# Performance work log

Hardware: AMD Instinct MI355X
Metric: run time of the kernel (lower is better)

## Reference

```python
import jax, jax.numpy as jnp
import numpy as np

B = 256      # number of graphs
IN = 128     # input_dim
FD = 256     # feature_dim (dims[1])
HID = 256    # hidden_dim of attention block (dims[2])
OUT = 128    # final output dim (dims[3])
TXT = 512    # text_emb_dim

LENGTHS = np.asarray(128 + (np.arange(B) % 256), dtype=np.int64)  # ragged lens 128..383
N = int(LENGTHS.sum())  # 65408 total nodes
LMAX = int(LENGTHS.max())  # 383


def setup_inputs() -> dict:
    key = jax.random.key(0)
    ks = jax.random.split(key, 16)
    s = 0.02
    return {
        "input": jax.random.normal(ks[0], (N, IN), jnp.float32),
        "text_emb": jax.random.normal(ks[1], (B, TXT), jnp.float32),
        "repeat_list": jnp.asarray(LENGTHS),
        # layer 0: Linear(IN -> FD)
        "W0": jax.random.normal(ks[2], (IN, FD), jnp.float32) * s,
        "b0": jax.random.normal(ks[3], (FD,), jnp.float32) * s,
        # cross-attention block params
        "Wq": jax.random.normal(ks[4], (TXT, FD), jnp.float32) * s,
        "bq": jax.random.normal(ks[5], (FD,), jnp.float32) * s,
        "Wk": jax.random.normal(ks[6], (FD, FD), jnp.float32) * s,
        "bk": jax.random.normal(ks[7], (FD,), jnp.float32) * s,
        "Wv": jax.random.normal(ks[8], (FD, FD), jnp.float32) * s,
        "bv": jax.random.normal(ks[9], (FD,), jnp.float32) * s,
        "Wo": jax.random.normal(ks[10], (FD, HID), jnp.float32) * s,
        "bo": jax.random.normal(ks[11], (HID,), jnp.float32) * s,
        # layer 2: Linear(HID -> OUT), last layer (no activation)
        "W2": jax.random.normal(ks[12], (HID, OUT), jnp.float32) * s,
        "b2": jax.random.normal(ks[13], (OUT,), jnp.float32) * s,
    }


def _cross_attention(h, text_emb, repeat_list, Wq, bq, Wk, bk, Wv, bv, Wo, bo):
    # h: [N, FD] packed ragged node features; repeat_list: [B] lengths (constant ints)
    n = h.shape[0]
    b = repeat_list.shape[0]
    fd = h.shape[1]
    # pad ragged -> [B, LMAX, FD] (pad value 0) + validity mask
    seg = jnp.repeat(jnp.arange(b), repeat_list, total_repeat_length=n)  # [N] graph id
    offsets = jnp.cumsum(repeat_list) - repeat_list                      # [B] start of each graph
    pos = jnp.arange(n) - offsets[seg]                                   # [N] within-graph pos
    padded = jnp.zeros((b, LMAX, fd), h.dtype).at[seg, pos].set(h)
    valid = jnp.arange(LMAX)[None, :] < repeat_list[:, None]             # [B, L]

    q = text_emb @ Wq + bq                              # [B, FD]
    k = (padded @ Wk + bk) * valid[..., None]           # masked_fill(mask==0, 0)
    v = (padded @ Wv + bv) * valid[..., None]

    # query is broadcast identically over the padded-length axis, so each row of the
    # [L, L] score matrix is the same vector: scores[b, j] = q[b] . k[b, j]
    scores = jnp.einsum('bf,bjf->bj', q, k)             # [B, L]
    scores = jnp.where(valid, scores, -jnp.inf)         # mask invalid columns j
    p = jax.nn.softmax(scores, axis=-1)                 # [B, L]
    # output = attention^T @ value with identical rows => out[b,j,:] = p[b,j] * sum_i v[b,i,:]
    v_sum = v.sum(axis=1)                               # [B, FD] (padded rows already zero)
    out_pad = p[..., None] * v_sum[:, None, :]          # [B, L, FD]
    out_nodes = out_pad[seg, pos]                       # unpad-concat -> [N, FD]
    return out_nodes @ Wo + bo                          # [N, HID]


def reference(input, text_emb, repeat_list, W0, b0, Wq, bq, Wk, bk, Wv, bv, Wo, bo, W2, b2):
    h = jax.nn.relu(input @ W0 + b0)                                     # layer 0 + relu
    h = _cross_attention(h, text_emb, repeat_list, Wq, bq, Wk, bk, Wv, bv, Wo, bo)
    h = jax.nn.relu(h)                                                   # layer 1 + relu
    return h @ W2 + b2                                                   # layer 2 (last, no act)
```

## Files before the change

### kernel.cpp

```cpp
#include <hip/hip_runtime.h>
#include <math.h>

#define B_G   256
#define IN_D  128
#define FD    256
#define HID   256
#define OUT_D 128
#define TXT   512
#define XKS   136

typedef short bf16x8 __attribute__((ext_vector_type(8)));
typedef float f32x4  __attribute__((ext_vector_type(4)));

__device__ __forceinline__ unsigned bf_rne(float x) {
    unsigned u = __float_as_uint(x);
    u += 0x7fffu + ((u >> 16) & 1u);
    return u >> 16;
}
__device__ __forceinline__ float bf_to_f(unsigned h) {
    return __uint_as_float(h << 16);
}
__device__ __forceinline__ void split2(float a0, float a1, unsigned& hp, unsigned& lp) {
    unsigned h0 = bf_rne(a0), h1 = bf_rne(a1);
    float r0 = a0 - bf_to_f(h0), r1 = a1 - bf_to_f(h1);
    hp = h0 | (h1 << 16);
    lp = bf_rne(r0) | (bf_rne(r1) << 16);
}

__global__ __launch_bounds__(256) void k_prepA(
    const float* __restrict__ text_emb, const float* __restrict__ Wq,
    const float* __restrict__ bq, const float* __restrict__ Wk,
    const float* __restrict__ W0, const float* __restrict__ W2,
    const int* __restrict__ lens,
    float* __restrict__ qk, int* __restrict__ offsets, float* __restrict__ hsum,
    unsigned short* __restrict__ W0sH, unsigned short* __restrict__ W0sL,
    unsigned short* __restrict__ W2sH, unsigned short* __restrict__ W2sL)
{
    int blk = blockIdx.x, t = threadIdx.x;
    __shared__ float te[TXT];
    __shared__ float q[FD];
    __shared__ int   sc[B_G];

    if (blk < 256) {
        int b = blk;
        hsum[b * FD + t] = 0.f;
        for (int i = t; i < TXT; i += 256) te[i] = text_emb[(size_t)b * TXT + i];
        __syncthreads();
        float acc = bq[t];
        for (int k = 0; k < TXT; k++) acc = fmaf(te[k], Wq[k * FD + t], acc);
        q[t] = acc;
        __syncthreads();
        float a2 = 0.f;
        for (int f = 0; f < FD; f++) a2 = fmaf(Wk[t * FD + f], q[f], a2);
        qk[b * FD + t] = a2;
    } else if (blk < 264) {
        int e = (blk - 256) * 256 + t;
        if (e < 1024) {
            int kc = e >> 8, c = e & 255;
            size_t base = (size_t)(kc * 256 + c) * 32;
            for (int kk = 0; kk < 32; kk++) {
                float v = W0[(size_t)(kc * 32 + kk) * FD + c];
                unsigned h = bf_rne(v);
                float r = v - bf_to_f(h);
                W0sH[base + kk] = (unsigned short)h;
                W0sL[base + kk] = (unsigned short)bf_rne(r);
            }
        } else {
            int e2 = e - 1024;
            int kc = e2 >> 7, c = e2 & 127;
            size_t base = (size_t)(kc * 128 + c) * 32;
            for (int kk = 0; kk < 32; kk++) {
                float v = W2[(size_t)(kc * 32 + kk) * OUT_D + c];
                unsigned h = bf_rne(v);
                float r = v - bf_to_f(h);
                W2sH[base + kk] = (unsigned short)h;
                W2sL[base + kk] = (unsigned short)bf_rne(r);
            }
        }
    } else {
        sc[t] = lens[t];
        __syncthreads();
        for (int d = 1; d < 256; d <<= 1) {
            int v = (t >= d) ? sc[t - d] : 0;
            __syncthreads();
            sc[t] += v;
            __syncthreads();
        }
        offsets[t + 1] = sc[t];
        if (t == 0) offsets[0] = 0;
    }
}

__global__ __launch_bounds__(256, 4) void k_l0_mfma(
    const float* __restrict__ X,
    const unsigned short* __restrict__ W0sH, const unsigned short* __restrict__ W0sL,
    const float* __restrict__ b0, const float* __restrict__ qk,
    const int* __restrict__ offsets,
    float* __restrict__ scores, float* __restrict__ hsum)
{
    int b = blockIdx.y;
    int off = offsets[b], len = offsets[b + 1] - off;
    int n0 = blockIdx.x * 64;
    if (n0 >= len) return;
    int nvalid = min(64, len - n0);

    __shared__ __align__(16) unsigned short XsH[64 * XKS], XsL[64 * XKS];
    __shared__ float qks[FD];
    __shared__ float bsh[FD];
    __shared__ float red[4][64];

    int tid = threadIdx.x;
    int lane = tid & 63, w = tid >> 6;
    int ln = lane & 15, quad = lane >> 4;

    qks[tid] = qk[b * FD + tid];
    bsh[tid] = b0[tid];

    {
        int node_s = tid >> 2, ks = (tid & 3) * 32;
        const float4* Xr4 = (const float4*)(X + (size_t)(off + n0 + node_s) * IN_D + ks);
        bool v = (node_s < nvalid);
#pragma unroll
        for (int g = 0; g < 4; g++) {
            float4 a, c4;
            if (v) { a = Xr4[2 * g]; c4 = Xr4[2 * g + 1]; }
            else   { a = make_float4(0.f, 0.f, 0.f, 0.f); c4 = a; }
            uint4 hq, lq;
            split2(a.x,  a.y,  hq.x, lq.x);
            split2(a.z,  a.w,  hq.y, lq.y);
            split2(c4.x, c4.y, hq.z, lq.z);
            split2(c4.z, c4.w, hq.w, lq.w);
            *(uint4*)&XsH[node_s * XKS + ks + g * 8] = hq;
            *(uint4*)&XsL[node_s * XKS + ks + g * 8] = lq;
        }
    }
    __syncthreads();

    f32x4 acc[4][4] = {};
#pragma unroll
    for (int kc = 0; kc < 4; kc++) {
        bf16x8 AH[4], AL[4];
#pragma unroll
        for (int i = 0; i < 4; i++) {
            AH[i] = *(const bf16x8*)&XsH[(16 * i + ln) * XKS + kc * 32 + quad * 8];
            AL[i] = *(const bf16x8*)&XsL[(16 * i + ln) * XKS + kc * 32 + quad * 8];
        }
#pragma unroll
        for (int j = 0; j < 4; j++) {
            int c = 64 * w + 16 * j + ln;
            size_t base = (size_t)(kc * 256 + c) * 32 + quad * 8;
            bf16x8 BH = *(const bf16x8*)&W0sH[base];
            bf16x8 BL = *(const bf16x8*)&W0sL[base];
#pragma unroll
            for (int i = 0; i < 4; i++) {
                acc[i][j] = __builtin_amdgcn_mfma_f32_16x16x32_bf16(AH[i], BH, acc[i][j], 0, 0, 0);
                acc[i][j] = __builtin_amdgcn_mfma_f32_16x16x32_bf16(AH[i], BL, acc[i][j], 0, 0, 0);
                acc[i][j] = __builtin_amdgcn_mfma_f32_16x16x32_bf16(AL[i], BH, acc[i][j], 0, 0, 0);
            }
        }
    }

    float sp[4][4];
    float cs[4] = {0.f, 0.f, 0.f, 0.f};
#pragma unroll
    for (int i = 0; i < 4; i++)
#pragma unroll
        for (int r = 0; r < 4; r++) sp[i][r] = 0.f;

#pragma unroll
    for (int i = 0; i < 4; i++)
#pragma unroll
        for (int j = 0; j < 4; j++) {
            int c = 64 * w + 16 * j + ln;
            float bb = bsh[c], qv = qks[c];
#pragma unroll
            for (int r = 0; r < 4; r++) {
                int node = 16 * i + 4 * quad + r;
                float h = acc[i][j][r] + bb;
                h = (h > 0.f && node < nvalid) ? h : 0.f;
                sp[i][r] = fmaf(h, qv, sp[i][r]);
                cs[j] += h;
            }
        }
#pragma unroll
    for (int i = 0; i < 4; i++)
#pragma unroll
        for (int r = 0; r < 4; r++) {
            float s = sp[i][r];
            s += __shfl_xor(s, 1); s += __shfl_xor(s, 2);
            s += __shfl_xor(s, 4); s += __shfl_xor(s, 8);
            sp[i][r] = s;
        }
    if (ln == 0) {
#pragma unroll
        for (int i = 0; i < 4; i++)
#pragma unroll
            for (int r = 0; r < 4; r++)
                red[w][16 * i + 4 * quad + r] = sp[i][r];
    }
#pragma unroll
    for (int j = 0; j < 4; j++) {
        float s = cs[j];
        s += __shfl_xor(s, 16); s += __shfl_xor(s, 32);
        if (quad == 0) atomicAdd(&hsum[b * FD + 64 * w + 16 * j + ln], s);
    }
    __syncthreads();
    if (tid < 64 && tid < nvalid)
        scores[off + n0 + tid] = red[0][tid] + red[1][tid] + red[2][tid] + red[3][tid];
}

__global__ __launch_bounds__(1024) void k_graph(
    const float* __restrict__ scores, const float* __restrict__ hsum,
    const float* __restrict__ Wv, const float* __restrict__ bv,
    const float* __restrict__ Wo, const int* __restrict__ offsets,
    float* __restrict__ wvec, float* __restrict__ smax, float* __restrict__ dinv)
{
    int b = blockIdx.x, tid = threadIdx.x;
    int t = tid & 255, g = tid >> 8;
    int off = offsets[b], len = offsets[b + 1] - off;
    __shared__ float redm[16], reds[16];
    __shared__ float hs[FD], vs[FD];
    __shared__ float part[4][FD];

    float m = -INFINITY;
    for (int i = tid; i < len; i += 1024) m = fmaxf(m, scores[off + i]);
    for (int d = 1; d < 64; d <<= 1) m = fmaxf(m, __shfl_xor(m, d));
    if ((tid & 63) == 0) redm[tid >> 6] = m;
    __syncthreads();
    m = -INFINITY;
#pragma unroll
    for (int k = 0; k < 16; k++) m = fmaxf(m, redm[k]);

    float s = 0.f;
    for (int i = tid; i < len; i += 1024) s += expf(scores[off + i] - m);
    for (int d = 1; d < 64; d <<= 1) s += __shfl_xor(s, d);
    if ((tid & 63) == 0) reds[tid >> 6] = s;
    if (g == 0) hs[t] = hsum[b * FD + t];
    __syncthreads();
    s = 0.f;
#pragma unroll
    for (int k = 0; k < 16; k++) s += reds[k];

    float acc = (g == 0) ? (float)len * bv[t] : 0.f;
    for (int f = 64 * g; f < 64 * g + 64; f++) acc = fmaf(hs[f], Wv[f * FD + t], acc);
    part[g][t] = acc;
    __syncthreads();
    if (g == 0) vs[t] = part[0][t] + part[1][t] + part[2][t] + part[3][t];
    __syncthreads();
    float a2 = 0.f;
    for (int f = 64 * g; f < 64 * g + 64; f++) a2 = fmaf(vs[f], Wo[f * HID + t], a2);
    part[g][t] = a2;
    __syncthreads();
    if (g == 0) wvec[b * HID + t] = part[0][t] + part[1][t] + part[2][t] + part[3][t];
    if (tid == 0) { smax[b] = m; dinv[b] = 1.0f / s; }
}

__global__ __launch_bounds__(256, 4) void k_fin_mfma(
    const float* __restrict__ scores, const float* __restrict__ wvec,
    const float* __restrict__ bo,
    const unsigned short* __restrict__ W2sH, const unsigned short* __restrict__ W2sL,
    const float* __restrict__ b2, const float* __restrict__ smax,
    const float* __restrict__ dinv, const int* __restrict__ offsets,
    float* __restrict__ Y)
{
    int b = blockIdx.y;
    int off = offsets[b], len = offsets[b + 1] - off;
    int n0 = blockIdx.x * 64;
    if (n0 >= len) return;
    int nvalid = min(64, len - n0);

    int tid = threadIdx.x;
    int lane = tid & 63, w = tid >> 6;
    int ln = lane & 15, quad = lane >> 4;

    __shared__ __align__(16) unsigned short ZsH[64 * XKS], ZsL[64 * XKS];
    __shared__ float ps[64];
    __shared__ float wsh[HID];
    __shared__ float bosh[HID];
    __shared__ float b2sh[OUT_D];

    wsh[tid] = wvec[b * HID + tid];
    bosh[tid] = bo[tid];
    if (tid < OUT_D) b2sh[tid] = b2[tid];
    if (tid < 64) {
        float p = 0.f;
        if (tid < nvalid) p = expf(scores[off + n0 + tid] - smax[b]) * dinv[b];
        ps[tid] = p;
    }
    __syncthreads();

    f32x4 acc[4][2] = {};
    int node_s = tid >> 2, ks = (tid & 3) * 32;

#pragma unroll
    for (int h = 0; h < 2; h++) {
        if (h) __syncthreads();
        {
            float pn = ps[node_s];
            int kg0 = h * 128 + ks;
#pragma unroll
            for (int g = 0; g < 4; g++) {
                uint4 hq, lq;
                int kb = kg0 + g * 8;
                float z0, z1;
                z0 = fmaxf(fmaf(pn, wsh[kb + 0], bosh[kb + 0]), 0.f);
                z1 = fmaxf(fmaf(pn, wsh[kb + 1], bosh[kb + 1]), 0.f);
                split2(z0, z1, hq.x, lq.x);
                z0 = fmaxf(fmaf(pn, wsh[kb + 2], bosh[kb + 2]), 0.f);
                z1 = fmaxf(fmaf(pn, wsh[kb + 3], bosh[kb + 3]), 0.f);
                split2(z0, z1, hq.y, lq.y);
                z0 = fmaxf(fmaf(pn, wsh[kb + 4], bosh[kb + 4]), 0.f);
                z1 = fmaxf(fmaf(pn, wsh[kb + 5], bosh[kb + 5]), 0.f);
                split2(z0, z1, hq.z, lq.z);
                z0 = fmaxf(fmaf(pn, wsh[kb + 6], bosh[kb + 6]), 0.f);
                z1 = fmaxf(fmaf(pn, wsh[kb + 7], bosh[kb + 7]), 0.f);
                split2(z0, z1, hq.w, lq.w);
                *(uint4*)&ZsH[node_s * XKS + ks + g * 8] = hq;
                *(uint4*)&ZsL[node_s * XKS + ks + g * 8] = lq;
            }
        }
        __syncthreads();

#pragma unroll
        for (int kc = 0; kc < 4; kc++) {
            bf16x8 AH[4], AL[4];
#pragma unroll
            for (int i = 0; i < 4; i++) {
                AH[i] = *(const bf16x8*)&ZsH[(16 * i + ln) * XKS + kc * 32 + quad * 8];
                AL[i] = *(const bf16x8*)&ZsL[(16 * i + ln) * XKS + kc * 32 + quad * 8];
            }
#pragma unroll
            for (int j = 0; j < 2; j++) {
                int c = 32 * w + 16 * j + ln;
                size_t base = (size_t)((h * 4 + kc) * 128 + c) * 32 + quad * 8;
                bf16x8 BH = *(const bf16x8*)&W2sH[base];
                bf16x8 BL = *(const bf16x8*)&W2sL[base];
#pragma unroll
                for (int i = 0; i < 4; i++) {
                    acc[i][j] = __builtin_amdgcn_mfma_f32_16x16x32_bf16(AH[i], BH, acc[i][j], 0, 0, 0);
                    acc[i][j] = __builtin_amdgcn_mfma_f32_16x16x32_bf16(AH[i], BL, acc[i][j], 0, 0, 0);
                    acc[i][j] = __builtin_amdgcn_mfma_f32_16x16x32_bf16(AL[i], BH, acc[i][j], 0, 0, 0);
                }
            }
        }
    }

#pragma unroll
    for (int i = 0; i < 4; i++)
#pragma unroll
        for (int j = 0; j < 2; j++) {
            int c = 32 * w + 16 * j + ln;
            float bb = b2sh[c];
#pragma unroll
            for (int r = 0; r < 4; r++) {
                int node = 16 * i + 4 * quad + r;
                if (node < nvalid)
                    Y[(size_t)(off + n0 + node) * OUT_D + c] = acc[i][j][r] + bb;
            }
        }
}

extern "C" void kernel_launch(void* const* d_in, const int* in_sizes, int n_in,
                              void* d_out, int out_size, void* d_ws, size_t ws_size,
                              hipStream_t stream)
{
    const float* X        = (const float*)d_in[0];
    const float* text_emb = (const float*)d_in[1];
    const int*   lens     = (const int*)d_in[2];
    const float* W0       = (const float*)d_in[3];
    const float* b0       = (const float*)d_in[4];
    const float* Wq       = (const float*)d_in[5];
    const float* bq       = (const float*)d_in[6];
    const float* Wk       = (const float*)d_in[7];
    const float* Wv       = (const float*)d_in[9];
    const float* bv       = (const float*)d_in[10];
    const float* Wo       = (const float*)d_in[11];
    const float* bo       = (const float*)d_in[12];
    const float* W2       = (const float*)d_in[13];
    const float* b2       = (const float*)d_in[14];
    float* Y = (float*)d_out;

    char* base = (char*)d_ws;
    size_t o = 0;
    int*   offsets = (int*)(base + o);            o += 1088;
    float* qkbuf   = (float*)(base + o);          o += 262144;
    float* wvecb   = (float*)(base + o);          o += 262144;
    float* smaxb   = (float*)(base + o);          o += 1024;
    float* dinvb   = (float*)(base + o);          o += 1024;
    float* hsum    = (float*)(base + o);          o += 262144;
    float* scores  = (float*)(base + o);          o += 262144;
    unsigned short* W0sH = (unsigned short*)(base + o); o += 65536;
    unsigned short* W0sL = (unsigned short*)(base + o); o += 65536;
    unsigned short* W2sH = (unsigned short*)(base + o); o += 65536;
    unsigned short* W2sL = (unsigned short*)(base + o); o += 65536;

    k_prepA<<<265, 256, 0, stream>>>(text_emb, Wq, bq, Wk, W0, W2, lens,
                                     qkbuf, offsets, hsum, W0sH, W0sL, W2sH, W2sL);
    k_l0_mfma<<<dim3(6, B_G), 256, 0, stream>>>(X, W0sH, W0sL, b0, qkbuf, offsets, scores, hsum);
    k_graph<<<B_G, 1024, 0, stream>>>(scores, hsum, Wv, bv, Wo, offsets, wvecb, smaxb, dinvb);
    k_fin_mfma<<<dim3(6, B_G), 256, 0, stream>>>(scores, wvecb, bo, W2sH, W2sL, b2, smaxb, dinvb, offsets, Y);
}
```

Measured before the change: 201.0 us.

## Fuse per-graph softmax/projection into layer-0 kernel via last-block counter

Drops the separate k_graph launch. Each graph's last-finishing layer-0 block, found through an atomic counter that k_prepA resets, now computes the softmax max and sum and the Wv/Wo projection with 256 threads. B-operand loads in both MFMA kernels are also software-prefetched one step ahead. This removes one kernel launch and its dependency gap. In exchange the tail work runs serially in one 256-thread block per graph instead of a 1024-thread block, and it needs thread fences and an extra counter buffer.

```diff
diff --git a/kernel.cpp b/kernel.cpp
--- a/kernel.cpp
+++ b/kernel.cpp
@@ -33,6 +33,7 @@
     const float* __restrict__ W0, const float* __restrict__ W2,
     const int* __restrict__ lens,
     float* __restrict__ qk, int* __restrict__ offsets, float* __restrict__ hsum,
+    int* __restrict__ cntr,
     unsigned short* __restrict__ W0sH, unsigned short* __restrict__ W0sL,
     unsigned short* __restrict__ W2sH, unsigned short* __restrict__ W2sL)
 {
@@ -44,6 +45,7 @@
     if (blk < 256) {
         int b = blk;
         hsum[b * FD + t] = 0.f;
+        if (t == 0) cntr[b] = 0;
         for (int i = t; i < TXT; i += 256) te[i] = text_emb[(size_t)b * TXT + i];
         __syncthreads();
         float acc = bq[t];
@@ -96,163 +98,174 @@
     const unsigned short* __restrict__ W0sH, const unsigned short* __restrict__ W0sL,
     const float* __restrict__ b0, const float* __restrict__ qk,
     const int* __restrict__ offsets,
-    float* __restrict__ scores, float* __restrict__ hsum)
+    const float* __restrict__ Wv, const float* __restrict__ bv,
+    const float* __restrict__ Wo,
+    float* __restrict__ scores, float* __restrict__ hsum,
+    int* __restrict__ cntr,
+    float* __restrict__ wvec, float* __restrict__ smax, float* __restrict__ dinv)
 {
     int b = blockIdx.y;
     int off = offsets[b], len = offsets[b + 1] - off;
     int n0 = blockIdx.x * 64;
-    if (n0 >= len) return;
-    int nvalid = min(64, len - n0);
 
     __shared__ __align__(16) unsigned short XsH[64 * XKS], XsL[64 * XKS];
     __shared__ float qks[FD];
     __shared__ float bsh[FD];
     __shared__ float red[4][64];
+    __shared__ float hs[FD], vs[FD];
+    __shared__ float redm[4], reds[4];
+    __shared__ int   isLast;
 
     int tid = threadIdx.x;
     int lane = tid & 63, w = tid >> 6;
     int ln = lane & 15, quad = lane >> 4;
 
-    qks[tid] = qk[b * FD + tid];
-    bsh[tid] = b0[tid];
+    if (n0 < len) {
+        int nvalid = min(64, len - n0);
+        qks[tid] = qk[b * FD + tid];
+        bsh[tid] = b0[tid];
+
+        {
+            int node_s = tid >> 2, ks = (tid & 3) * 32;
+            const float4* Xr4 = (const float4*)(X + (size_t)(off + n0 + node_s) * IN_D + ks);
+            bool v = (node_s < nvalid);
+#pragma unroll
+            for (int g = 0; g < 4; g++) {
+                float4 a, c4;
+                if (v) { a = Xr4[2 * g]; c4 = Xr4[2 * g + 1]; }
+                else   { a = make_float4(0.f, 0.f, 0.f, 0.f); c4 = a; }
+                uint4 hq, lq;
+                split2(a.x,  a.y,  hq.x, lq.x);
+                split2(a.z,  a.w,  hq.y, lq.y);
+                split2(c4.x, c4.y, hq.z, lq.z);
+                split2(c4.z, c4.w, hq.w, lq.w);
+                *(uint4*)&XsH[node_s * XKS + ks + g * 8] = hq;
+                *(uint4*)&XsL[node_s * XKS + ks + g * 8] = lq;
+            }
+        }
+        __syncthreads();
+
+        f32x4 acc[4][4] = {};
+#pragma unroll
+        for (int kc = 0; kc < 4; kc++) {
+            bf16x8 AH[4], AL[4];
+#pragma unroll
+            for (int i = 0; i < 4; i++) {
+                AH[i] = *(const bf16x8*)&XsH[(16 * i + ln) * XKS + kc * 32 + quad * 8];
+                AL[i] = *(const bf16x8*)&XsL[(16 * i + ln) * XKS + kc * 32 + quad * 8];
+            }
+            bf16x8 BH, BL;
+            {
+                int c = 64 * w + ln;
+                size_t base = (size_t)(kc * 256 + c) * 32 + quad * 8;
+                BH = *(const bf16x8*)&W0sH[base];
+                BL = *(const bf16x8*)&W0sL[base];
+            }
+#pragma unroll
+            for (int j = 0; j < 4; j++) {
+                bf16x8 BHn, BLn;
+                if (j < 3) {
+                    int c = 64 * w + 16 * (j + 1) + ln;
+                    size_t base = (size_t)(kc * 256 + c) * 32 + quad * 8;
+                    BHn = *(const bf16x8*)&W0sH[base];
+                    BLn = *(const bf16x8*)&W0sL[base];
+                }
+#pragma unroll
+                for (int i = 0; i < 4; i++) {
+                    acc[i][j] = __builtin_amdgcn_mfma_f32_16x16x32_bf16(AH[i], BH, acc[i][j], 0, 0, 0);
+                    acc[i][j] = __builtin_amdgcn_mfma_f32_16x16x32_bf16(AH[i], BL, acc[i][j], 0, 0, 0);
+                    acc[i][j] = __builtin_amdgcn_mfma_f32_16x16x32_bf16(AL[i], BH, acc[i][j], 0, 0, 0);
+                }
+                BH = BHn; BL = BLn;
+            }
+        }
+
+        float sp[4][4];
+        float cs[4] = {0.f, 0.f, 0.f, 0.f};
+#pragma unroll
+        for (int i = 0; i < 4; i++)
+#pragma unroll
+            for (int r = 0; r < 4; r++) sp[i][r] = 0.f;
+
+#pragma unroll
+        for (int i = 0; i < 4; i++)
+#pragma unroll
+            for (int j = 0; j < 4; j++) {
+                int c = 64 * w + 16 * j + ln;
+                float bb = bsh[c], qv = qks[c];
+#pragma unroll
+                for (int r = 0; r < 4; r++) {
+                    int node = 16 * i + 4 * quad + r;
+                    float h = acc[i][j][r] + bb;
+                    h = (h > 0.f && node < nvalid) ? h : 0.f;
+                    sp[i][r] = fmaf(h, qv, sp[i][r]);
+                    cs[j] += h;
+                }
+            }
+#pragma unroll
+        for (int i = 0; i < 4; i++)
+#pragma unroll
+            for (int r = 0; r < 4; r++) {
+                float s = sp[i][r];
+                s += __shfl_xor(s, 1); s += __shfl_xor(s, 2);
+                s += __shfl_xor(s, 4); s += __shfl_xor(s, 8);
+                sp[i][r] = s;
+            }
+        if (ln == 0) {
+#pragma unroll
+            for (int i = 0; i < 4; i++)
+#pragma unroll
+                for (int r = 0; r < 4; r++)
+                    red[w][16 * i + 4 * quad + r] = sp[i][r];
+        }
+#pragma unroll
+        for (int j = 0; j < 4; j++) {
+            float s = cs[j];
+            s += __shfl_xor(s, 16); s += __shfl_xor(s, 32);
+            if (quad == 0) atomicAdd(&hsum[b * FD + 64 * w + 16 * j + ln], s);
+        }
+        __syncthreads();
+        if (tid < 64 && tid < nvalid)
+            scores[off + n0 + tid] = red[0][tid] + red[1][tid] + red[2][tid] + red[3][tid];
+    }
+
+    __threadfence();
+    __syncthreads();
+    if (tid == 0) {
+        int prev = atomicAdd(&cntr[b], 1);
+        isLast = (prev == 5);
+    }
+    __syncthreads();
+    if (!isLast) return;
+    __threadfence();
 
     {
-        int node_s = tid >> 2, ks = (tid & 3) * 32;
-        const float4* Xr4 = (const float4*)(X + (size_t)(off + n0 + node_s) * IN_D + ks);
-        bool v = (node_s < nvalid);
-#pragma unroll
-        for (int g = 0; g < 4; g++) {
-            float4 a, c4;
-            if (v) { a = Xr4[2 * g]; c4 = Xr4[2 * g + 1]; }
-            else   { a = make_float4(0.f, 0.f, 0.f, 0.f); c4 = a; }
-            uint4 hq, lq;
-            split2(a.x,  a.y,  hq.x, lq.x);
-            split2(a.z,  a.w,  hq.y, lq.y);
-            split2(c4.x, c4.y, hq.z, lq.z);
-            split2(c4.z, c4.w, hq.w, lq.w);
-            *(uint4*)&XsH[node_s * XKS + ks + g * 8] = hq;
-            *(uint4*)&XsL[node_s * XKS + ks + g * 8] = lq;
-        }
-    }
-    __syncthreads();
-
-    f32x4 acc[4][4] = {};
-#pragma unroll
-    for (int kc = 0; kc < 4; kc++) {
-        bf16x8 AH[4], AL[4];
-#pragma unroll
-        for (int i = 0; i < 4; i++) {
-            AH[i] = *(const bf16x8*)&XsH[(16 * i + ln) * XKS + kc * 32 + quad * 8];
-            AL[i] = *(const bf16x8*)&XsL[(16 * i + ln) * XKS + kc * 32 + quad * 8];
-        }
-#pragma unroll
-        for (int j = 0; j < 4; j++) {
-            int c = 64 * w + 16 * j + ln;
-            size_t base = (size_t)(kc * 256 + c) * 32 + quad * 8;
-            bf16x8 BH = *(const bf16x8*)&W0sH[base];
-            bf16x8 BL = *(const bf16x8*)&W0sL[base];
-#pragma unroll
-            for (int i = 0; i < 4; i++) {
-                acc[i][j] = __builtin_amdgcn_mfma_f32_16x16x32_bf16(AH[i], BH, acc[i][j], 0, 0, 0);
-                acc[i][j] = __builtin_amdgcn_mfma_f32_16x16x32_bf16(AH[i], BL, acc[i][j], 0, 0, 0);
-                acc[i][j] = __builtin_amdgcn_mfma_f32_16x16x32_bf16(AL[i], BH, acc[i][j], 0, 0, 0);
-            }
-        }
-    }
-
-    float sp[4][4];
-    float cs[4] = {0.f, 0.f, 0.f, 0.f};
-#pragma unroll
-    for (int i = 0; i < 4; i++)
-#pragma unroll
-        for (int r = 0; r < 4; r++) sp[i][r] = 0.f;
-
-#pragma unroll
-    for (int i = 0; i < 4; i++)
-#pragma unroll
-        for (int j = 0; j < 4; j++) {
-            int c = 64 * w + 16 * j + ln;
-            float bb = bsh[c], qv = qks[c];
-#pragma unroll
-            for (int r = 0; r < 4; r++) {
-                int node = 16 * i + 4 * quad + r;
-                float h = acc[i][j][r] + bb;
-                h = (h > 0.f && node < nvalid) ? h : 0.f;
-                sp[i][r] = fmaf(h, qv, sp[i][r]);
-                cs[j] += h;
-            }
-        }
-#pragma unroll
-    for (int i = 0; i < 4; i++)
-#pragma unroll
-        for (int r = 0; r < 4; r++) {
-            float s = sp[i][r];
-            s += __shfl_xor(s, 1); s += __shfl_xor(s, 2);
-            s += __shfl_xor(s, 4); s += __shfl_xor(s, 8);
-            sp[i][r] = s;
-        }
-    if (ln == 0) {
-#pragma unroll
-        for (int i = 0; i < 4; i++)
-#pragma unroll
-            for (int r = 0; r < 4; r++)
-                red[w][16 * i + 4 * quad + r] = sp[i][r];
-    }
-#pragma unroll
-    for (int j = 0; j < 4; j++) {
-        float s = cs[j];
-        s += __shfl_xor(s, 16); s += __shfl_xor(s, 32);
-        if (quad == 0) atomicAdd(&hsum[b * FD + 64 * w + 16 * j + ln], s);
-    }
-    __syncthreads();
-    if (tid < 64 && tid < nvalid)
-        scores[off + n0 + tid] = red[0][tid] + red[1][tid] + red[2][tid] + red[3][tid];
-}
-
-__global__ __launch_bounds__(1024) void k_graph(
-    const float* __restrict__ scores, const float* __restrict__ hsum,
-    const float* __restrict__ Wv, const float* __restrict__ bv,
-    const float* __restrict__ Wo, const int* __restrict__ offsets,
-    float* __restrict__ wvec, float* __restrict__ smax, float* __restrict__ dinv)
-{
-    int b = blockIdx.x, tid = threadIdx.x;
-    int t = tid & 255, g = tid >> 8;
-    int off = offsets[b], len = offsets[b + 1] - off;
-    __shared__ float redm[16], reds[16];
-    __shared__ float hs[FD], vs[FD];
-    __shared__ float part[4][FD];
-
-    float m = -INFINITY;
-    for (int i = tid; i < len; i += 1024) m = fmaxf(m, scores[off + i]);
-    for (int d = 1; d < 64; d <<= 1) m = fmaxf(m, __shfl_xor(m, d));
-    if ((tid & 63) == 0) redm[tid >> 6] = m;
-    __syncthreads();
-    m = -INFINITY;
-#pragma unroll
-    for (int k = 0; k < 16; k++) m = fmaxf(m, redm[k]);
-
-    float s = 0.f;
-    for (int i = tid; i < len; i += 1024) s += expf(scores[off + i] - m);
-    for (int d = 1; d < 64; d <<= 1) s += __shfl_xor(s, d);
-    if ((tid & 63) == 0) reds[tid >> 6] = s;
-    if (g == 0) hs[t] = hsum[b * FD + t];
-    __syncthreads();
-    s = 0.f;
-#pragma unroll
-    for (int k = 0; k < 16; k++) s += reds[k];
-
-    float acc = (g == 0) ? (float)len * bv[t] : 0.f;
-    for (int f = 64 * g; f < 64 * g + 64; f++) acc = fmaf(hs[f], Wv[f * FD + t], acc);
-    part[g][t] = acc;
-    __syncthreads();
-    if (g == 0) vs[t] = part[0][t] + part[1][t] + part[2][t] + part[3][t];
-    __syncthreads();
-    float a2 = 0.f;
-    for (int f = 64 * g; f < 64 * g + 64; f++) a2 = fmaf(vs[f], Wo[f * HID + t], a2);
-    part[g][t] = a2;
-    __syncthreads();
-    if (g == 0) wvec[b * HID + t] = part[0][t] + part[1][t] + part[2][t] + part[3][t];
-    if (tid == 0) { smax[b] = m; dinv[b] = 1.0f / s; }
+        float m = -INFINITY;
+        for (int i = tid; i < len; i += 256) m = fmaxf(m, scores[off + i]);
+#pragma unroll
+        for (int d = 1; d < 64; d <<= 1) m = fmaxf(m, __shfl_xor(m, d));
+        if (lane == 0) redm[w] = m;
+        hs[tid] = hsum[b * FD + tid];
+        __syncthreads();
+        m = fmaxf(fmaxf(redm[0], redm[1]), fmaxf(redm[2], redm[3]));
+
+        float s = 0.f;
+        for (int i = tid; i < len; i += 256) s += expf(scores[off + i] - m);
+#pragma unroll
+        for (int d = 1; d < 64; d <<= 1) s += __shfl_xor(s, d);
+        if (lane == 0) reds[w] = s;
+        __syncthreads();
+        s = reds[0] + reds[1] + reds[2] + reds[3];
+
+        float acc = (float)len * bv[tid];
+        for (int f = 0; f < FD; f++) acc = fmaf(hs[f], Wv[f * FD + tid], acc);
+        vs[tid] = acc;
+        __syncthreads();
+        float a2 = 0.f;
+        for (int f = 0; f < HID; f++) a2 = fmaf(vs[f], Wo[f * HID + tid], a2);
+        wvec[b * HID + tid] = a2;
+        if (tid == 0) { smax[b] = m; dinv[b] = 1.0f / s; }
+    }
 }
 
 __global__ __launch_bounds__(256, 4) void k_fin_mfma(
@@ -321,6 +334,14 @@
         }
         __syncthreads();
 
+        bf16x8 BH[2], BL[2];
+#pragma unroll
+        for (int j = 0; j < 2; j++) {
+            int c = 32 * w + 16 * j + ln;
+            size_t base = (size_t)((h * 4) * 128 + c) * 32 + quad * 8;
+            BH[j] = *(const bf16x8*)&W2sH[base];
+            BL[j] = *(const bf16x8*)&W2sL[base];
+        }
 #pragma unroll
         for (int kc = 0; kc < 4; kc++) {
             bf16x8 AH[4], AL[4];
@@ -329,19 +350,27 @@
                 AH[i] = *(const bf16x8*)&ZsH[(16 * i + ln) * XKS + kc * 32 + quad * 8];
                 AL[i] = *(const bf16x8*)&ZsL[(16 * i + ln) * XKS + kc * 32 + quad * 8];
             }
+            bf16x8 BHn[2], BLn[2];
+            if (kc < 3) {
+#pragma unroll
+                for (int j = 0; j < 2; j++) {
+                    int c = 32 * w + 16 * j + ln;
+                    size_t base = (size_t)((h * 4 + kc + 1) * 128 + c) * 32 + quad * 8;
+                    BHn[j] = *(const bf16x8*)&W2sH[base];
+                    BLn[j] = *(const bf16x8*)&W2sL[base];
+                }
+            }
 #pragma unroll
             for (int j = 0; j < 2; j++) {
-                int c = 32 * w + 16 * j + ln;
-                size_t base = (size_t)((h * 4 + kc) * 128 + c) * 32 + quad * 8;
-                bf16x8 BH = *(const bf16x8*)&W2sH[base];
-                bf16x8 BL = *(const bf16x8*)&W2sL[base];
 #pragma unroll
                 for (int i = 0; i < 4; i++) {
-                    acc[i][j] = __builtin_amdgcn_mfma_f32_16x16x32_bf16(AH[i], BH, acc[i][j], 0, 0, 0);
-                    acc[i][j] = __builtin_amdgcn_mfma_f32_16x16x32_bf16(AH[i], BL, acc[i][j], 0, 0, 0);
-                    acc[i][j] = __builtin_amdgcn_mfma_f32_16x16x32_bf16(AL[i], BH, acc[i][j], 0, 0, 0);
+                    acc[i][j] = __builtin_amdgcn_mfma_f32_16x16x32_bf16(AH[i], BH[j], acc[i][j], 0, 0, 0);
+                    acc[i][j] = __builtin_amdgcn_mfma_f32_16x16x32_bf16(AH[i], BL[j], acc[i][j], 0, 0, 0);
+                    acc[i][j] = __builtin_amdgcn_mfma_f32_16x16x32_bf16(AL[i], BH[j], acc[i][j], 0, 0, 0);
                 }
             }
+#pragma unroll
+            for (int j = 0; j < 2; j++) { BH[j] = BHn[j]; BL[j] = BLn[j]; }
         }
     }
 
@@ -389,14 +418,17 @@
     float* dinvb   = (float*)(base + o);          o += 1024;
     float* hsum    = (float*)(base + o);          o += 262144;
     float* scores  = (float*)(base + o);          o += 262144;
+    int*   cntr    = (int*)(base + o);            o += 1024;
     unsigned short* W0sH = (unsigned short*)(base + o); o += 65536;
     unsigned short* W0sL = (unsigned short*)(base + o); o += 65536;
     unsigned short* W2sH = (unsigned short*)(base + o); o += 65536;
     unsigned short* W2sL = (unsigned short*)(base + o); o += 65536;
 
     k_prepA<<<265, 256, 0, stream>>>(text_emb, Wq, bq, Wk, W0, W2, lens,
-                                     qkbuf, offsets, hsum, W0sH, W0sL, W2sH, W2sL);
-    k_l0_mfma<<<dim3(6, B_G), 256, 0, stream>>>(X, W0sH, W0sL, b0, qkbuf, offsets, scores, hsum);
-    k_graph<<<B_G, 1024, 0, stream>>>(scores, hsum, Wv, bv, Wo, offsets, wvecb, smaxb, dinvb);
-    k_fin_mfma<<<dim3(6, B_G), 256, 0, stream>>>(scores, wvecb, bo, W2sH, W2sL, b2, smaxb, dinvb, offsets, Y);
-}
+                                     qkbuf, offsets, hsum, cntr, W0sH, W0sL, W2sH, W2sL);
+    k_l0_mfma<<<dim3(6, B_G), 256, 0, stream>>>(X, W0sH, W0sL, b0, qkbuf, offsets,
+                                                Wv, bv, Wo, scores, hsum, cntr,
+                                                wvecb, smaxb, dinvb);
+    k_fin_mfma<<<dim3(6, B_G), 256, 0, stream>>>(scores, wvecb, bo, W2sH, W2sL, b2,
+                                                 smaxb, dinvb, offsets, Y);
+}
```

After: 347.4 us. 72.8% more time.
